# Optimization experiments

Measured on AMD Instinct MI355X. Metric: run time of the kernel, lower is better.

The kernel has to match this reference:

```python
import jax, jax.numpy as jnp
import numpy as np
from jax import lax

TOPN = 4
CAT_NUM = 4
NUM_CLS = 200
PAD = 224
IMG = 448
HP = IMG + 2 * PAD  # 896
CROP = 224
IOU_THRESH = 0.25


def _gen_edge_anchors():
    # generate_default_anchor_maps: 3 pyramid levels; anchors ordered (anchor, h, w)
    # per level to match the channel-first flatten of ProposalNet tidy outputs.
    settings = [
        (32, 48.0, [2 ** (1. / 3.), 2 ** (2. / 3.)], [0.667, 1.0, 1.5]),
        (64, 96.0, [2 ** (1. / 3.), 2 ** (2. / 3.)], [0.667, 1.0, 1.5]),
        (128, 192.0, [1.0, 2 ** (1. / 3.), 2 ** (2. / 3.)], [0.667, 1.0, 1.5]),
    ]
    blocks = []
    for stride, size, scales, ars in settings:
        n = int(np.ceil(IMG / stride))
        c = np.arange(n, dtype=np.float64) * stride + stride / 2.0
        cy, cx = np.meshgrid(c, c, indexing='ij')
        for sc in scales:
            for ar in ars:
                h = size * sc / np.sqrt(ar)
                w = size * sc * np.sqrt(ar)
                a = np.stack([cy - h / 2., cx - w / 2., cy + h / 2., cx + w / 2.], axis=-1)
                blocks.append(a.reshape(-1, 4))
    e = np.concatenate(blocks, axis=0)  # [1614, 4] (y0,x0,y1,x1)
    return (e + PAD).astype(np.int32)   # offset into padded image, truncated to int


EDGE_ANCHORS = _gen_edge_anchors()


def _conv(x, w, b, stride, pad):
    y = lax.conv_general_dilated(x, w, (stride, stride), [(pad, pad), (pad, pad)],
                                 dimension_numbers=('NCHW', 'OIHW', 'NCHW'))
    return y + b[None, :, None, None]


def _proposal_net(x, d1w, d1b, d2w, d2b, d3w, d3b, t1w, t1b, t2w, t2b, t3w, t3b):
    B = x.shape[0]
    d1 = jax.nn.relu(_conv(x, d1w, d1b, 1, 1))   # [B,128,14,14]
    d2 = jax.nn.relu(_conv(d1, d2w, d2b, 2, 1))  # [B,128,7,7]
    d3 = jax.nn.relu(_conv(d2, d3w, d3b, 2, 1))  # [B,128,4,4]
    t1 = _conv(d1, t1w, t1b, 1, 0).reshape(B, -1)  # 6*14*14 = 1176
    t2 = _conv(d2, t2w, t2b, 1, 0).reshape(B, -1)  # 6*7*7  = 294
    t3 = _conv(d3, t3w, t3b, 1, 0).reshape(B, -1)  # 9*4*4  = 144
    return jnp.concatenate([t1, t2, t3], axis=1)   # [B,1614]


def _hard_nms(scores, boxes, area):
    # Greedy hard NMS over A anchors, returns TOPN kept indices (score-desc order).
    A = scores.shape[0]

    def body(k, carry):
        mask, idxs = carry
        i = jnp.argmax(jnp.where(mask, scores, -jnp.inf))
        b = boxes[i]
        yy0 = jnp.maximum(boxes[:, 0], b[0])
        xx0 = jnp.maximum(boxes[:, 1], b[1])
        yy1 = jnp.minimum(boxes[:, 2], b[2])
        xx1 = jnp.minimum(boxes[:, 3], b[3])
        inter = jnp.maximum(yy1 - yy0, 0.) * jnp.maximum(xx1 - xx0, 0.)
        iou = inter / (area + area[i] - inter)
        mask = (mask & (iou < IOU_THRESH)).at[i].set(False)
        return mask, idxs.at[k].set(i.astype(jnp.int32))

    _, idxs = lax.fori_loop(0, TOPN, body, (jnp.ones((A,), bool), jnp.zeros((TOPN,), jnp.int32)))
    return idxs


def _crop_resize(img, box):
    # img [3,HP,HP], box [4] float (integer-valued). Bilinear, align_corners=True:
    # src coord = y0 + i*(h-1)/(CROP-1) over the slice [y0:y1).
    y0, x0, y1, x1 = box[0], box[1], box[2], box[3]
    t = jnp.arange(CROP, dtype=jnp.float32) / (CROP - 1.)
    ys = y0 + t * (y1 - y0 - 1.)
    xs = x0 + t * (x1 - x0 - 1.)
    yi0 = jnp.clip(jnp.floor(ys).astype(jnp.int32), 0, HP - 1)
    xi0 = jnp.clip(jnp.floor(xs).astype(jnp.int32), 0, HP - 1)
    yi1 = jnp.minimum(yi0 + 1, HP - 1)
    xi1 = jnp.minimum(xi0 + 1, HP - 1)
    wy = (ys - yi0.astype(jnp.float32))[None, :, None]
    wx = (xs - xi0.astype(jnp.float32))[None, None, :]
    r0 = img[:, yi0, :]
    r1 = img[:, yi1, :]
    rows = r0 + (r1 - r0) * wy          # [3,CROP,HP]
    c0 = rows[:, :, xi0]
    c1 = rows[:, :, xi1]
    return c0 + (c1 - c0) * wx          # [3,CROP,CROP]


def reference(x, rpn_feature, feature, resnet_out,
              down1_w, down1_b, down2_w, down2_b, down3_w, down3_b,
              tidy1_w, tidy1_b, tidy2_w, tidy2_b, tidy3_w, tidy3_b,
              feat_w, feat_b, partcls_w, partcls_b, concat_w, concat_b):
    B = x.shape[0]
    boxes_f = jnp.asarray(EDGE_ANCHORS, jnp.float32)
    area = (boxes_f[:, 2] - boxes_f[:, 0]) * (boxes_f[:, 3] - boxes_f[:, 1])

    rpn_score = _proposal_net(lax.stop_gradient(rpn_feature),
                              down1_w, down1_b, down2_w, down2_b, down3_w, down3_b,
                              tidy1_w, tidy1_b, tidy2_w, tidy2_b, tidy3_w, tidy3_b)
    scores_sg = lax.stop_gradient(rpn_score)
    top_idx = jax.vmap(lambda s: _hard_nms(s, boxes_f, area))(scores_sg)   # [B,TOPN]
    top_n_prob = jnp.take_along_axis(rpn_score, top_idx, axis=1)           # [B,TOPN]

    x_pad = jnp.pad(x, ((0, 0), (0, 0), (PAD, PAD), (PAD, PAD)))           # [B,3,896,896]
    sel_boxes = boxes_f[top_idx]                                           # [B,TOPN,4]
    part_imgs = jax.vmap(lambda img, bxs: jax.vmap(lambda b: _crop_resize(img, b))(bxs))(x_pad, sel_boxes)
    part_imgs = lax.stop_gradient(part_imgs).reshape(B * TOPN, 3, CROP, CROP)  # detach()

    # per-crop feature trunk (stand-in for shared ResNet50): strided 7x7 conv + GAP
    pf = jax.nn.relu(_conv(part_imgs, feat_w, feat_b, 32, 3)).mean(axis=(2, 3))  # [B*TOPN,2048]
    part_logits = (pf @ partcls_w.T + partcls_b).reshape(B, TOPN, NUM_CLS)
    part_feature = pf.reshape(B, TOPN, -1)[:, :CAT_NUM].reshape(B, -1)           # [B,4*2048]
    concat_out = jnp.concatenate([part_feature, feature], axis=1)                # [B,10240]
    concat_logits = concat_out @ concat_w.T + concat_b
    return resnet_out, concat_logits, part_logits, top_idx, top_n_prob


def setup_inputs():
    key = jax.random.key(0)
    ks = jax.random.split(key, 13)
    B = 16
    n = lambda k, shp, s=1.0: jax.random.normal(k, shp, jnp.float32) * s
    z = lambda c: jnp.zeros((c,), jnp.float32)
    return {
        'x': n(ks[0], (B, 3, 448, 448)),
        'rpn_feature': jax.nn.relu(n(ks[1], (B, 2048, 14, 14))),
        'feature': n(ks[2], (B, 2048)),
        'resnet_out': n(ks[3], (B, 200)),
        'down1_w': n(ks[4], (128, 2048, 3, 3), 0.01),
        'down1_b': z(128),
        'down2_w': n(ks[5], (128, 128, 3, 3), 0.03),
        'down2_b': z(128),
        'down3_w': n(ks[6], (128, 128, 3, 3), 0.03),
        'down3_b': z(128),
        'tidy1_w': n(ks[7], (6, 128, 1, 1), 0.1),
        'tidy1_b': z(6),
        'tidy2_w': n(ks[8], (6, 128, 1, 1), 0.1),
        'tidy2_b': z(6),
        'tidy3_w': n(ks[9], (9, 128, 1, 1), 0.1),
        'tidy3_b': z(9),
        'feat_w': n(ks[10], (2048, 3, 7, 7), 0.05),
        'feat_b': z(2048),
        'partcls_w': n(ks[11], (200, 2048), 0.02),
        'partcls_b': z(200),
        'concat_w': n(ks[12], (200, 2048 * (CAT_NUM + 1)), 0.01),
        'concat_b': z(200),
    }
```

## Files before the change

### kernel.cpp

```cpp
#include <hip/hip_runtime.h>
#include <math.h>

#define NANCH 1614
#define A1 1176
#define A2 1470
#define KSPLIT 4
#define N_D1E (16*128*196)

#define OFF_D1 0
#define OFF_D2 401408
#define OFF_D3 501760
#define OFF_SC 534528
#define OFF_PF 560352
#define OFF_P  691424
#define OFF_INT 1152416
#define OFF_BIG 1158944
#define SZ_AT 3211264
#define SZ_BW 1179648
#define OFF_ATH (OFF_BIG)
#define OFF_ATL (OFF_ATH + SZ_AT)
#define OFF_BWH (OFF_ATL + SZ_AT)
#define OFF_BWL (OFF_BWH + SZ_BW)
#define OFF_PM  (OFF_BWL + SZ_BW)
#define SZ_PM   3612672
#define TOTAL_MFMA_F (OFF_PM + SZ_PM)
#define N_D2E (16*128*49)
#define N_D3E (16*128*16)
#define OFF_P2 OFF_BIG
#define OFF_P3 (OFF_BIG + 4*N_D2E)

#define OUT_CONCAT 3200
#define OUT_PART   6400
#define OUT_TIDX   19200
#define OUT_TPROB  19264

typedef __attribute__((ext_vector_type(8))) short short8;
typedef __attribute__((ext_vector_type(4))) float f32x4;

__device__ __forceinline__ unsigned short bf16_rn(float f) {
    unsigned u = __float_as_uint(f);
    unsigned r = u + 0x7fffu + ((u >> 16) & 1u);
    return (unsigned short)(r >> 16);
}
__device__ __forceinline__ float bf16_to_f(unsigned short h) {
    return __uint_as_float(((unsigned)h) << 16);
}

__global__ void anchor_kernel(int* __restrict__ anc) {
    int i = blockIdx.x * 256 + threadIdx.x;
    if (i >= NANCH) return;
    int stride, n, sgroup, j;
    double size;
    if (i < A1)      { stride = 32;  size = 48.0;  n = 14; j = i;      sgroup = 0; }
    else if (i < A2) { stride = 64;  size = 96.0;  n = 7;  j = i - A1; sgroup = 0; }
    else             { stride = 128; size = 192.0; n = 4;  j = i - A2; sgroup = 1; }
    int cells = n * n;
    int combo = j / cells, cell = j % cells;
    int sc_i = combo / 3, ar_i = combo % 3;
    double sc;
    if (sgroup == 0) sc = pow(2.0, (double)(sc_i + 1) / 3.0);
    else             sc = (sc_i == 0) ? 1.0 : pow(2.0, (double)sc_i / 3.0);
    double ar = (ar_i == 0) ? 0.667 : ((ar_i == 1) ? 1.0 : 1.5);
    int y = cell / n, x = cell % n;
    double cy = (double)y * stride + stride / 2.0;
    double cx = (double)x * stride + stride / 2.0;
    double sq = sqrt(ar);
    double h = size * sc / sq, w = size * sc * sq;
    anc[i*4+0] = (int)(cy - h/2.0 + 224.0);
    anc[i*4+1] = (int)(cx - w/2.0 + 224.0);
    anc[i*4+2] = (int)(cy + h/2.0 + 224.0);
    anc[i*4+3] = (int)(cx + w/2.0 + 224.0);
}

__launch_bounds__(256)
__global__ void split_rpn_t(const float* __restrict__ rpn,
                            unsigned short* __restrict__ ath, unsigned short* __restrict__ atl) {
    __shared__ float T[32*197];
    int b = blockIdx.x >> 6, icb = blockIdx.x & 63;
    int tid = threadIdx.x;
    for (int idx = tid; idx < 32*196; idx += 256) {
        int i = idx / 196, s = idx % 196;
        T[i*197 + s] = rpn[((size_t)(b*2048 + icb*32 + i))*196 + s];
    }
    __syncthreads();
    for (int idx = tid; idx < 32*196; idx += 256) {
        int s = idx >> 5, i = idx & 31;
        float f = T[i*197 + s];
        unsigned short hi = bf16_rn(f);
        unsigned short lo = bf16_rn(f - bf16_to_f(hi));
        size_t o = ((size_t)(b*196 + s))*2048 + icb*32 + i;
        ath[o] = hi; atl[o] = lo;
    }
}

__global__ void split_w(const float* __restrict__ w1,
                        unsigned short* __restrict__ bwh, unsigned short* __restrict__ bwl) {
    int idx = blockIdx.x * 256 + threadIdx.x;
    if (idx >= 9*128*2048) return;
    int tap = idx / (128*2048);
    int rem = idx % (128*2048);
    int oc = rem >> 11, ic = rem & 2047;
    float f = w1[((size_t)(oc*2048 + ic))*9 + tap];
    unsigned short hi = bf16_rn(f);
    unsigned short lo = bf16_rn(f - bf16_to_f(hi));
    bwh[idx] = hi; bwl[idx] = lo;
}

#define ABUF (64*40)
#define BBUF (128*40)
__launch_bounds__(256)
__global__ void d1_mfma(const unsigned short* __restrict__ ath, const unsigned short* __restrict__ atl,
                        const unsigned short* __restrict__ bwh, const unsigned short* __restrict__ bwl,
                        float* __restrict__ partM) {
    __shared__ unsigned short Ah[2*ABUF], Al[2*ABUF], Bh[2*BBUF], Bl[2*BBUF];
    int tid = threadIdx.x;
    int tap = blockIdx.x / 49, mb = blockIdx.x % 49;
    int dy = tap/3 - 1, dx = tap%3 - 1;
    int wave = tid >> 6, lane = tid & 63;
    int wr = wave >> 1, wc = wave & 1;
    int lg = lane >> 4, lr = lane & 15;

    const unsigned short* asrc[2]; unsigned short* adst[2]; bool avalid[2];
#pragma unroll
    for (int rep = 0; rep < 2; ++rep) {
        int idx = rep*256 + tid;
        int rw = idx >> 3, half = (idx >> 2) & 1, slot = idx & 3;
        int grow = mb*64 + rw;
        int b = grow / 196, s = grow % 196;
        int y = s / 14, x = s % 14;
        int ys = y + dy, xs = x + dx;
        bool av = (ys >= 0) && (ys < 14) && (xs >= 0) && (xs < 14);
        avalid[rep] = av;
        asrc[rep] = (half ? atl : ath)
            + ((size_t)(b*196 + (av ? (ys*14 + xs) : 0)))*2048 + slot*8;
        adst[rep] = (half ? Al : Ah) + rw*40 + slot*8;
    }
    const unsigned short* bsrc[4]; unsigned short* bdst[4];
#pragma unroll
    for (int rep = 0; rep < 4; ++rep) {
        int idx = rep*256 + tid;
        int oc = idx >> 3, half = (idx >> 2) & 1, slot = idx & 3;
        bsrc[rep] = (half ? bwl : bwh) + ((size_t)(tap*128 + oc))*2048 + slot*8;
        bdst[rep] = (half ? Bl : Bh) + oc*40 + slot*8;
    }

    f32x4 acc[2][4];
#pragma unroll
    for (int r2 = 0; r2 < 2; ++r2)
#pragma unroll
        for (int f = 0; f < 4; ++f) acc[r2][f] = (f32x4){0.f, 0.f, 0.f, 0.f};
    const short8 zer = {0,0,0,0,0,0,0,0};

    short8 ga[2], gb[4];
#pragma unroll
    for (int rep = 0; rep < 2; ++rep) ga[rep] = avalid[rep] ? *(const short8*)(asrc[rep]) : zer;
#pragma unroll
    for (int rep = 0; rep < 4; ++rep) gb[rep] = *(const short8*)(bsrc[rep]);
#pragma unroll
    for (int rep = 0; rep < 2; ++rep) *(short8*)(adst[rep]) = ga[rep];
#pragma unroll
    for (int rep = 0; rep < 4; ++rep) *(short8*)(bdst[rep]) = gb[rep];
    __syncthreads();

    int abase_w = wr*32*40 + lr*40 + lg*8;
    int bbase_w = wc*64*40 + lg*8;

    for (int step = 0; step < 64; ++step) {
        int buf = step & 1;
        if (step + 1 < 64) {
            int ic0 = (step + 1) * 32;
#pragma unroll
            for (int rep = 0; rep < 2; ++rep) ga[rep] = avalid[rep] ? *(const short8*)(asrc[rep] + ic0) : zer;
#pragma unroll
            for (int rep = 0; rep < 4; ++rep) gb[rep] = *(const short8*)(bsrc[rep] + ic0);
        }
        int ab = buf*ABUF, bb = buf*BBUF;
        short8 ah0 = *(const short8*)&Ah[ab + abase_w];
        short8 ah1 = *(const short8*)&Ah[ab + abase_w + 16*40];
        short8 al0 = *(const short8*)&Al[ab + abase_w];
        short8 al1 = *(const short8*)&Al[ab + abase_w + 16*40];
#pragma unroll
        for (int f = 0; f < 4; ++f) {
            int bo = bb + bbase_w + (f*16 + lr)*40;
            short8 b_h = *(const short8*)&Bh[bo];
            short8 b_l = *(const short8*)&Bl[bo];
            acc[0][f] = __builtin_amdgcn_mfma_f32_16x16x32_bf16(ah0, b_h, acc[0][f], 0, 0, 0);
            acc[0][f] = __builtin_amdgcn_mfma_f32_16x16x32_bf16(ah0, b_l, acc[0][f], 0, 0, 0);
            acc[0][f] = __builtin_amdgcn_mfma_f32_16x16x32_bf16(al0, b_h, acc[0][f], 0, 0, 0);
            acc[1][f] = __builtin_amdgcn_mfma_f32_16x16x32_bf16(ah1, b_h, acc[1][f], 0, 0, 0);
            acc[1][f] = __builtin_amdgcn_mfma_f32_16x16x32_bf16(ah1, b_l, acc[1][f], 0, 0, 0);
            acc[1][f] = __builtin_amdgcn_mfma_f32_16x16x32_bf16(al1, b_h, acc[1][f], 0, 0, 0);
        }
        if (step + 1 < 64) {
            int nb = buf ^ 1;
#pragma unroll
            for (int rep = 0; rep < 2; ++rep) *(short8*)(adst[rep] + nb*ABUF) = ga[rep];
#pragma unroll
            for (int rep = 0; rep < 4; ++rep) *(short8*)(bdst[rep] + nb*BBUF) = gb[rep];
        }
        __syncthreads();
    }
#pragma unroll
    for (int r2 = 0; r2 < 2; ++r2)
#pragma unroll
    for (int f = 0; f < 4; ++f) {
        int oc = wc*64 + f*16 + lr;
#pragma unroll
        for (int r = 0; r < 4; ++r) {
            int row = mb*64 + wr*32 + r2*16 + lg*4 + r;
            partM[((size_t)tap*3136 + row)*128 + oc] = acc[r2][f][r];
        }
    }
}

__global__ void d1_combine(const float* __restrict__ partM, const float* __restrict__ b1,
                           float* __restrict__ d1) {
    int idx = blockIdx.x*256 + threadIdx.x;
    if (idx >= 3136*128) return;
    int oc = idx & 127, row = idx >> 7;
    float s = 0.f;
#pragma unroll
    for (int t = 0; t < 9; ++t) s += partM[(size_t)t*3136*128 + idx];
    int b = row / 196, sp = row % 196;
    d1[(b*128 + oc)*196 + sp] = fmaxf(s + b1[oc], 0.f);
}

__launch_bounds__(256)
__global__ void conv_d1_part(const float* __restrict__ rpn, const float* __restrict__ w1,
                             float* __restrict__ part) {
    __shared__ float lin[8*256];
    __shared__ float lwT[576];
    int tid = threadIdx.x;
    int ks = blockIdx.x & 3;
    int tile = (blockIdx.x >> 2) & 15;
    int b = blockIdx.x >> 6;
    int py = tid >> 4, px = tid & 15;
    bool pvalid = (py >= 1) && (py <= 14) && (px >= 1) && (px <= 14);
    int in_off = (b*2048)*196 + (py-1)*14 + (px-1);
    const float* wb = w1 + tile*8*18432;
    int s = tid, y = s / 14, x = s % 14;
    bool active = s < 196;
    float acc[8];
#pragma unroll
    for (int o = 0; o < 8; ++o) acc[o] = 0.f;
    float pv[8]; float wv[3];
    int c0 = ks * 64;
#pragma unroll
    for (int i = 0; i < 8; ++i) pv[i] = pvalid ? rpn[in_off + (c0*8 + i)*196] : 0.f;
#pragma unroll
    for (int r = 0; r < 3; ++r) {
        int u = tid + r*256;
        if (u < 576) { int oc = u/72, rem = u%72; wv[r] = wb[oc*18432 + c0*72 + rem]; }
    }
    for (int c = 0; c < 64; ++c) {
#pragma unroll
        for (int i = 0; i < 8; ++i) lin[i*256 + tid] = pv[i];
#pragma unroll
        for (int r = 0; r < 3; ++r) {
            int u = tid + r*256;
            if (u < 576) { int oc = u/72, rem = u%72; lwT[rem*8 + oc] = wv[r]; }
        }
        __syncthreads();
        if (c + 1 < 64) {
            int icb = (c0 + c + 1) * 8;
#pragma unroll
            for (int i = 0; i < 8; ++i) pv[i] = pvalid ? rpn[in_off + (icb + i)*196] : 0.f;
#pragma unroll
            for (int r = 0; r < 3; ++r) {
                int u = tid + r*256;
                if (u < 576) { int oc = u/72, rem = u%72; wv[r] = wb[oc*18432 + icb*9 + rem]; }
            }
        }
        if (active) {
#pragma unroll
            for (int ic = 0; ic < 8; ++ic) {
                int base = ic*256 + y*16 + x;
                float p[9];
                p[0]=lin[base+0];  p[1]=lin[base+1];  p[2]=lin[base+2];
                p[3]=lin[base+16]; p[4]=lin[base+17]; p[5]=lin[base+18];
                p[6]=lin[base+32]; p[7]=lin[base+33]; p[8]=lin[base+34];
#pragma unroll
                for (int k = 0; k < 9; ++k) {
                    const float4 wa  = *(const float4*)&lwT[(ic*9 + k)*8];
                    const float4 wb4 = *(const float4*)&lwT[(ic*9 + k)*8 + 4];
                    acc[0] += p[k]*wa.x;  acc[1] += p[k]*wa.y;
                    acc[2] += p[k]*wa.z;  acc[3] += p[k]*wa.w;
                    acc[4] += p[k]*wb4.x; acc[5] += p[k]*wb4.y;
                    acc[6] += p[k]*wb4.z; acc[7] += p[k]*wb4.w;
                }
            }
        }
        __syncthreads();
    }
    if (active) {
#pragma unroll
        for (int o = 0; o < 8; ++o) {
            int oc = tile*8 + o;
            part[ks*N_D1E + (b*128 + oc)*196 + s] = acc[o];
        }
    }
}

__global__ void d1_reduce(const float* __restrict__ part, const float* __restrict__ b1,
                          float* __restrict__ d1) {
    int idx = blockIdx.x * 256 + threadIdx.x;
    if (idx >= N_D1E) return;
    int oc = (idx / 196) & 127;
    float s = part[idx] + part[idx + N_D1E] + part[idx + 2*N_D1E] + part[idx + 3*N_D1E];
    d1[idx] = fmaxf(s + b1[oc], 0.f);
}

__launch_bounds__(256)
__global__ void conv_d2_part(const float* __restrict__ d1, const float* __restrict__ w2,
                             float* __restrict__ part) {
    __shared__ float lin[8*320];
    __shared__ float lwT[72*32];
    int tid = threadIdx.x;
    int ks = blockIdx.x & 3;
    int octile = (blockIdx.x >> 2) & 3;
    int b = blockIdx.x >> 4;
    int py = tid >> 4, px = tid & 15;
    bool pvalid = (py >= 1) && (py <= 14) && (px >= 1) && (px <= 14);
    int in_base = (b*128)*196 + (py-1)*14 + (px-1);
    int g = tid >> 6, s = tid & 63;
    int yo = s / 7, xo = s % 7;
    bool active = s < 49;
    const float* wb = w2 + (octile*32)*1152 + ks*288;

    float acc[8];
#pragma unroll
    for (int o = 0; o < 8; ++o) acc[o] = 0.f;
    float pv[8], wv[9];
#pragma unroll
    for (int i = 0; i < 8; ++i) pv[i] = pvalid ? d1[in_base + (ks*32 + i)*196] : 0.f;
#pragma unroll
    for (int r = 0; r < 9; ++r) {
        int u = tid + r*256; int oc_l = u/72, rem = u%72;
        wv[r] = wb[oc_l*1152 + rem];
    }
    for (int c = 0; c < 4; ++c) {
#pragma unroll
        for (int i = 0; i < 8; ++i) lin[i*320 + py*20 + px] = pv[i];
#pragma unroll
        for (int r = 0; r < 9; ++r) {
            int u = tid + r*256; int oc_l = u/72, rem = u%72;
            lwT[rem*32 + oc_l] = wv[r];
        }
        __syncthreads();
        if (c + 1 < 4) {
            int ic0 = ks*32 + (c+1)*8;
#pragma unroll
            for (int i = 0; i < 8; ++i) pv[i] = pvalid ? d1[in_base + (ic0 + i)*196] : 0.f;
#pragma unroll
            for (int r = 0; r < 9; ++r) {
                int u = tid + r*256; int oc_l = u/72, rem = u%72;
                wv[r] = wb[oc_l*1152 + (c+1)*72 + rem];
            }
        }
        if (active) {
#pragma unroll
            for (int ic = 0; ic < 8; ++ic) {
                int base = ic*320 + (2*yo)*20 + 2*xo;
                float p[9];
                p[0]=lin[base+0];  p[1]=lin[base+1];  p[2]=lin[base+2];
                p[3]=lin[base+20]; p[4]=lin[base+21]; p[5]=lin[base+22];
                p[6]=lin[base+40]; p[7]=lin[base+41]; p[8]=lin[base+42];
#pragma unroll
                for (int k = 0; k < 9; ++k) {
                    const float4 wa  = *(const float4*)&lwT[(ic*9 + k)*32 + g*8];
                    const float4 wb4 = *(const float4*)&lwT[(ic*9 + k)*32 + g*8 + 4];
                    acc[0] += p[k]*wa.x;  acc[1] += p[k]*wa.y;
                    acc[2] += p[k]*wa.z;  acc[3] += p[k]*wa.w;
                    acc[4] += p[k]*wb4.x; acc[5] += p[k]*wb4.y;
                    acc[6] += p[k]*wb4.z; acc[7] += p[k]*wb4.w;
                }
            }
        }
        __syncthreads();
    }
    if (active) {
#pragma unroll
        for (int o = 0; o < 8; ++o) {
            int oc = octile*32 + g*8 + o;
            part[ks*N_D2E + (b*128 + oc)*49 + s] = acc[o];
        }
    }
}

__launch_bounds__(256)
__global__ void conv_d3_part(const float* __restrict__ d2, const float* __restrict__ w3,
                             float* __restrict__ part) {
    __shared__ float lin3[8*108];
    __shared__ float lwT3[72*128];
    int tid = threadIdx.x;
    int ks = blockIdx.x & 15;
    int b = blockIdx.x >> 4;
    int g = tid >> 4, s = tid & 15;
    int yo = s >> 2, xo = s & 3;

    for (int r = 0; r < 4; ++r) {
        int u = tid + r*256;
        if (u < 864) {
            int ic = u / 108, rem = u % 108;
            int ty = rem / 12, tx = rem % 12;
            int iy = ty - 1, ix = tx - 1;
            float v = 0.f;
            if (iy >= 0 && iy < 7 && ix >= 0 && ix < 7)
                v = d2[(b*128 + ks*8 + ic)*49 + iy*7 + ix];
            lin3[u] = v;
        }
    }
#pragma unroll
    for (int r = 0; r < 36; ++r) {
        int u = tid + r*256;
        int oc_l = u / 72, rem = u % 72;
        lwT3[rem*128 + oc_l] = w3[oc_l*1152 + ks*72 + rem];
    }
    __syncthreads();

    float acc[8];
#pragma unroll
    for (int o = 0; o < 8; ++o) acc[o] = 0.f;
#pragma unroll
    for (int ic = 0; ic < 8; ++ic) {
        int base = ic*108 + (2*yo)*12 + 2*xo;
        float p[9];
        p[0]=lin3[base+0];  p[1]=lin3[base+1];  p[2]=lin3[base+2];
        p[3]=lin3[base+12]; p[4]=lin3[base+13]; p[5]=lin3[base+14];
        p[6]=lin3[base+24]; p[7]=lin3[base+25]; p[8]=lin3[base+26];
#pragma unroll
        for (int k = 0; k < 9; ++k) {
            const float4 wa  = *(const float4*)&lwT3[(ic*9 + k)*128 + g*8];
            const float4 wb4 = *(const float4*)&lwT3[(ic*9 + k)*128 + g*8 + 4];
            acc[0] += p[k]*wa.x;  acc[1] += p[k]*wa.y;
            acc[2] += p[k]*wa.z;  acc[3] += p[k]*wa.w;
            acc[4] += p[k]*wb4.x; acc[5] += p[k]*wb4.y;
            acc[6] += p[k]*wb4.z; acc[7] += p[k]*wb4.w;
        }
    }
#pragma unroll
    for (int o = 0; o < 8; ++o) {
        int oc = g*8 + o;
        part[ks*N_D3E + (b*128 + oc)*16 + s] = acc[o];
    }
}

__global__ void reduce_relu(const float* __restrict__ part, const float* __restrict__ bias,
                            float* __restrict__ out, int nsplit, int N, int SP) {
    int idx = blockIdx.x*256 + threadIdx.x;
    if (idx >= N) return;
    int oc = (idx / SP) & 127;
    float s = 0.f;
    for (int p = 0; p < nsplit; ++p) s += part[p*N + idx];
    out[idx] = fmaxf(s + bias[oc], 0.f);
}

__global__ void tidy_kernel(const float* __restrict__ d1, const float* __restrict__ d2, const float* __restrict__ d3,
                            const float* __restrict__ t1w, const float* __restrict__ t1b,
                            const float* __restrict__ t2w, const float* __restrict__ t2b,
                            const float* __restrict__ t3w, const float* __restrict__ t3b,
                            float* __restrict__ scores) {
    int idx = blockIdx.x * 256 + threadIdx.x;
    if (idx >= 16*NANCH) return;
    int b = idx / NANCH, i = idx % NANCH;
    const float* src; const float* tw; const float* tb; int S, c, s;
    if (i < A1)      { c = i/196;           s = i%196;        src = d1 + b*128*196 + s; S = 196; tw = t1w; tb = t1b; }
    else if (i < A2) { int j = i - A1; c = j/49; s = j%49;    src = d2 + b*128*49  + s; S = 49;  tw = t2w; tb = t2b; }
    else             { int j = i - A2; c = j/16; s = j%16;    src = d3 + b*128*16  + s; S = 16;  tw = t3w; tb = t3b; }
    float acc = tb[c];
    const float* wr = tw + c*128;
    for (int ic = 0; ic < 128; ++ic) acc += src[ic*S] * wr[ic];
    scores[idx] = acc;
}

__launch_bounds__(256)
__global__ void nms_kernel(const float* __restrict__ scores, const int* __restrict__ anc,
                           int* __restrict__ topidx, float* __restrict__ out) {
    __shared__ float s[NANCH];
    __shared__ float by0[NANCH], bx0[NANCH], by1[NANCH], bx1[NANCH], ar[NANCH];
    __shared__ float rv[256]; __shared__ int ri[256];
    __shared__ int sel[4];
    int b = blockIdx.x, tid = threadIdx.x;
    for (int j = tid; j < NANCH; j += 256) {
        s[j] = scores[b*NANCH + j];
        float y0 = (float)anc[j*4+0], x0 = (float)anc[j*4+1];
        float y1 = (float)anc[j*4+2], x1 = (float)anc[j*4+3];
        by0[j] = y0; bx0[j] = x0; by1[j] = y1; bx1[j] = x1;
        ar[j] = (y1 - y0) * (x1 - x0);
    }
    __syncthreads();
    for (int k = 0; k < 4; ++k) {
        float bv = -INFINITY; int bi = NANCH;
        for (int j = tid; j < NANCH; j += 256) {
            float v = s[j];
            if (v > bv) { bv = v; bi = j; }
        }
        rv[tid] = bv; ri[tid] = bi;
        __syncthreads();
        for (int off = 128; off > 0; off >>= 1) {
            if (tid < off) {
                float v2 = rv[tid+off]; int i2 = ri[tid+off];
                if (v2 > rv[tid] || (v2 == rv[tid] && i2 < ri[tid])) { rv[tid] = v2; ri[tid] = i2; }
            }
            __syncthreads();
        }
        int i = ri[0];
        if (tid == 0) sel[k] = i;
        float a0 = by0[i], a1 = bx0[i], a2 = by1[i], a3 = bx1[i], ai = ar[i];
        for (int j = tid; j < NANCH; j += 256) {
            float yy0 = fmaxf(by0[j], a0), xx0 = fmaxf(bx0[j], a1);
            float yy1 = fminf(by1[j], a2), xx1 = fminf(bx1[j], a3);
            float inter = fmaxf(yy1 - yy0, 0.f) * fmaxf(xx1 - xx0, 0.f);
            float iou = inter / (ar[j] + ai - inter);
            if (!(iou < 0.25f)) s[j] = -INFINITY;
        }
        if (tid == 0) s[i] = -INFINITY;
        __syncthreads();
    }
    if (tid < 4) {
        int i = sel[tid];
        topidx[b*4 + tid] = i;
        out[OUT_TIDX  + b*4 + tid] = (float)i;
        out[OUT_TPROB + b*4 + tid] = scores[b*NANCH + i];
    }
}

__device__ __forceinline__ float fetchpix(const float* img, int Y, int X) {
    if (Y >= 224 && Y < 672 && X >= 224 && X < 672) return img[(Y - 224)*448 + (X - 224)];
    return 0.f;
}

__global__ void sampler_kernel(const float* __restrict__ x, const int* __restrict__ anc,
                               const int* __restrict__ topidx, float* __restrict__ P) {
    int crop = blockIdx.x >> 2;
    int b = crop >> 2;
    int idx = topidx[crop];
    float y0 = (float)anc[idx*4+0], x0 = (float)anc[idx*4+1];
    float y1 = (float)anc[idx*4+2], x1 = (float)anc[idx*4+3];
    float dy = y1 - y0 - 1.0f, dx = x1 - x0 - 1.0f;
    const float* imgb = x + b*3*448*448;
    for (int u = (blockIdx.x & 3)*256 + threadIdx.x; u < 7203; u += 1024) {
        int c = u / 2401; int rem = u % 2401;
        int rid = rem / 49, cid = rem % 49;
        int oy = rid/7, ky = rid%7, ox = cid/7, kx = cid%7;
        int rr = 32*oy - 3 + ky, cc = 32*ox - 3 + kx;
        float val = 0.f;
        if (rr >= 0 && cc >= 0) {
            float ty = (float)rr / 223.0f;
            float ys = __fadd_rn(y0, __fmul_rn(ty, dy));
            int yi0 = (int)floorf(ys); yi0 = yi0 < 0 ? 0 : (yi0 > 895 ? 895 : yi0);
            int yi1 = (yi0 + 1 > 895) ? 895 : yi0 + 1;
            float wy = ys - (float)yi0;
            float tx = (float)cc / 223.0f;
            float xs = __fadd_rn(x0, __fmul_rn(tx, dx));
            int xi0 = (int)floorf(xs); xi0 = xi0 < 0 ? 0 : (xi0 > 895 ? 895 : xi0);
            int xi1 = (xi0 + 1 > 895) ? 895 : xi0 + 1;
            float wx = xs - (float)xi0;
            const float* img = imgb + c*448*448;
            float p00 = fetchpix(img, yi0, xi0), p10 = fetchpix(img, yi1, xi0);
            float p01 = fetchpix(img, yi0, xi1), p11 = fetchpix(img, yi1, xi1);
            float r0 = p00 + (p10 - p00)*wy;
            float r1 = p01 + (p11 - p01)*wy;
            val = r0 + (r1 - r0)*wx;
        }
        int pos = oy*7 + ox, kk = c*49 + ky*7 + kx;
        P[crop*7203 + pos*147 + kk] = val;
    }
}

__launch_bounds__(256)
__global__ void feat_gemm_kernel(const float* __restrict__ P, const float* __restrict__ fw,
                                 const float* __restrict__ fb, float* __restrict__ pf) {
    __shared__ float lp[49*148];
    int crop = blockIdx.x >> 3, tile = blockIdx.x & 7;
    int oc = tile*256 + threadIdx.x;
    for (int u = threadIdx.x; u < 7203; u += 256)
        lp[(u/147)*148 + (u%147)] = P[crop*7203 + u];
    __syncthreads();
    float s[49];
#pragma unroll
    for (int p = 0; p < 49; ++p) s[p] = 0.f;
    const float* wr = fw + oc*147;
    for (int kc = 0; kc < 36; ++kc) {
        float w0 = wr[kc*4], w1 = wr[kc*4+1], w2 = wr[kc*4+2], w3 = wr[kc*4+3];
#pragma unroll
        for (int p = 0; p < 49; ++p) {
            float4 v = *(const float4*)&lp[p*148 + kc*4];
            s[p] += v.x*w0 + v.y*w1 + v.z*w2 + v.w*w3;
        }
    }
    {
        float w0 = wr[144], w1 = wr[145], w2 = wr[146];
#pragma unroll
        for (int p = 0; p < 49; ++p)
            s[p] += lp[p*148+144]*w0 + lp[p*148+145]*w1 + lp[p*148+146]*w2;
    }
    float bias = fb[oc], acc = 0.f;
#pragma unroll
    for (int p = 0; p < 49; ++p) acc += fmaxf(s[p] + bias, 0.f);
    pf[crop*2048 + oc] = acc / 49.0f;
}

__global__ void partcls_kernel(const float* __restrict__ pf, const float* __restrict__ pw,
                               const float* __restrict__ pb, float* __restrict__ out) {
    int o = blockIdx.x; int crop = o / 200, cls = o % 200;
    int lane = threadIdx.x;
    const float* a = pf + crop*2048; const float* w = pw + cls*2048;
    float sum = 0.f;
#pragma unroll
    for (int i = 0; i < 8; ++i) {
        int k = lane*4 + i*256;
        float4 a4 = *(const float4*)&a[k];
        float4 w4 = *(const float4*)&w[k];
        sum += a4.x*w4.x + a4.y*w4.y + a4.z*w4.z + a4.w*w4.w;
    }
#pragma unroll
    for (int off = 32; off > 0; off >>= 1) sum += __shfl_down(sum, off);
    if (lane == 0) out[OUT_PART + o] = sum + pb[cls];
}

__launch_bounds__(256)
__global__ void concat_kernel(const float* __restrict__ pf, const float* __restrict__ feature,
                              const float* __restrict__ cw, const float* __restrict__ cb,
                              float* __restrict__ out) {
    __shared__ float red[4][16];
    int j = blockIdx.x, tid = threadIdx.x;
    const float* w = cw + (size_t)j*10240;
    float acc[16];
#pragma unroll
    for (int b = 0; b < 16; ++b) acc[b] = 0.f;
    for (int k = tid; k < 10240; k += 256) {
        float wk = w[k];
        const float* v; int stride;
        if (k < 8192) { v = pf + k; stride = 8192; }
        else          { v = feature + (k - 8192); stride = 2048; }
#pragma unroll
        for (int b = 0; b < 16; ++b) acc[b] += v[b*stride] * wk;
    }
#pragma unroll
    for (int b = 0; b < 16; ++b) {
        float s2 = acc[b];
#pragma unroll
        for (int off = 32; off > 0; off >>= 1) s2 += __shfl_down(s2, off);
        if ((tid & 63) == 0) red[tid >> 6][b] = s2;
    }
    __syncthreads();
    if (tid < 16)
        out[OUT_CONCAT + tid*200 + j] = red[0][tid] + red[1][tid] + red[2][tid] + red[3][tid] + cb[j];
}

extern "C" void kernel_launch(void* const* d_in, const int* in_sizes, int n_in,
                              void* d_out, int out_size, void* d_ws, size_t ws_size,
                              hipStream_t stream) {
    const float* x    = (const float*)d_in[0];
    const float* rpn  = (const float*)d_in[1];
    const float* feat = (const float*)d_in[2];
    const float* rout = (const float*)d_in[3];
    const float* d1w  = (const float*)d_in[4];
    const float* d1b  = (const float*)d_in[5];
    const float* d2w  = (const float*)d_in[6];
    const float* d2b  = (const float*)d_in[7];
    const float* d3w  = (const float*)d_in[8];
    const float* d3b  = (const float*)d_in[9];
    const float* t1w  = (const float*)d_in[10];
    const float* t1b  = (const float*)d_in[11];
    const float* t2w  = (const float*)d_in[12];
    const float* t2b  = (const float*)d_in[13];
    const float* t3w  = (const float*)d_in[14];
    const float* t3b  = (const float*)d_in[15];
    const float* fw   = (const float*)d_in[16];
    const float* fbb  = (const float*)d_in[17];
    const float* pw   = (const float*)d_in[18];
    const float* pb   = (const float*)d_in[19];
    const float* cw   = (const float*)d_in[20];
    const float* cb   = (const float*)d_in[21];
    float* out = (float*)d_out;
    float* wsf = (float*)d_ws;
    float* d1  = wsf + OFF_D1;
    float* d2  = wsf + OFF_D2;
    float* d3  = wsf + OFF_D3;
    float* sc  = wsf + OFF_SC;
    float* pfb = wsf + OFF_PF;
    float* P   = wsf + OFF_P;
    int* anc    = (int*)(wsf + OFF_INT);
    int* topidx = anc + NANCH*4;

    hipMemcpyAsync(out, rout, 3200*sizeof(float), hipMemcpyDeviceToDevice, stream);

    anchor_kernel<<<7, 256, 0, stream>>>(anc);

    bool use_mfma = ws_size >= (size_t)TOTAL_MFMA_F * sizeof(float);
    if (use_mfma) {
        unsigned short* ath = (unsigned short*)(wsf + OFF_ATH);
        unsigned short* atl = (unsigned short*)(wsf + OFF_ATL);
        unsigned short* bwh = (unsigned short*)(wsf + OFF_BWH);
        unsigned short* bwl = (unsigned short*)(wsf + OFF_BWL);
        float* pm = wsf + OFF_PM;
        split_rpn_t<<<1024, 256, 0, stream>>>(rpn, ath, atl);
        split_w<<<9216, 256, 0, stream>>>(d1w, bwh, bwl);
        d1_mfma<<<441, 256, 0, stream>>>(ath, atl, bwh, bwl, pm);
        d1_combine<<<(3136*128 + 255)/256, 256, 0, stream>>>(pm, d1b, d1);
    } else {
        float* part = wsf + OFF_BIG;
        conv_d1_part<<<16*16*KSPLIT, 256, 0, stream>>>(rpn, d1w, part);
        d1_reduce<<<(N_D1E + 255)/256, 256, 0, stream>>>(part, d1b, d1);
    }

    float* part2 = wsf + OFF_P2;
    float* part3 = wsf + OFF_P3;
    conv_d2_part<<<256, 256, 0, stream>>>(d1, d2w, part2);
    reduce_relu<<<(N_D2E + 255)/256, 256, 0, stream>>>(part2, d2b, d2, 4, N_D2E, 49);
    conv_d3_part<<<256, 256, 0, stream>>>(d2, d3w, part3);
    reduce_relu<<<(N_D3E + 255)/256, 256, 0, stream>>>(part3, d3b, d3, 16, N_D3E, 16);

    tidy_kernel<<<101, 256, 0, stream>>>(d1, d2, d3, t1w, t1b, t2w, t2b, t3w, t3b, sc);
    nms_kernel<<<16, 256, 0, stream>>>(sc, anc, topidx, out);
    sampler_kernel<<<256, 256, 0, stream>>>(x, anc, topidx, P);
    feat_gemm_kernel<<<512, 256, 0, stream>>>(P, fw, fbb, pfb);
    partcls_kernel<<<12800, 64, 0, stream>>>(pfb, pw, pb, out);
    concat_kernel<<<200, 256, 0, stream>>>(pfb, feat, cw, cb, out);
}
```

Baseline: 391.4 us.

## Port feature-conv GEMM to split-bf16 MFMA and swizzle d1 LDS layout

```diff
diff --git a/kernel.cpp b/kernel.cpp
--- a/kernel.cpp
+++ b/kernel.cpp
@@ -24,6 +24,10 @@
 #define OFF_PM  (OFF_BWL + SZ_BW)
 #define SZ_PM   3612672
 #define TOTAL_MFMA_F (OFF_PM + SZ_PM)
+#define OFF_BFH OFF_PM
+#define OFF_BFL (OFF_PM + 163840)
+#define OFF_PH  (OFF_PM + 327680)
+#define OFF_PL  (OFF_PM + 327680 + 250880)
 #define N_D2E (16*128*49)
 #define N_D3E (16*128*16)
 #define OFF_P2 OFF_BIG
@@ -106,19 +110,23 @@
     bwh[idx] = hi; bwl[idx] = lo;
 }
 
-#define ABUF (64*40)
-#define BBUF (128*40)
+#define ABUF 2048
+#define BBUF 4096
 __launch_bounds__(256)
 __global__ void d1_mfma(const unsigned short* __restrict__ ath, const unsigned short* __restrict__ atl,
                         const unsigned short* __restrict__ bwh, const unsigned short* __restrict__ bwl,
                         float* __restrict__ partM) {
     __shared__ unsigned short Ah[2*ABUF], Al[2*ABUF], Bh[2*BBUF], Bl[2*BBUF];
     int tid = threadIdx.x;
-    int tap = blockIdx.x / 49, mb = blockIdx.x % 49;
+    int q = blockIdx.x >> 3;
+    int tap = q / 7, g = q % 7;
+    int mb = g*8 + (blockIdx.x & 7);
+    if (mb >= 49) return;
     int dy = tap/3 - 1, dx = tap%3 - 1;
     int wave = tid >> 6, lane = tid & 63;
     int wr = wave >> 1, wc = wave & 1;
     int lg = lane >> 4, lr = lane & 15;
+    int ksw = (lg ^ (lr & 3)) << 3;
 
     const unsigned short* asrc[2]; unsigned short* adst[2]; bool avalid[2];
 #pragma unroll
@@ -133,7 +141,7 @@
         avalid[rep] = av;
         asrc[rep] = (half ? atl : ath)
             + ((size_t)(b*196 + (av ? (ys*14 + xs) : 0)))*2048 + slot*8;
-        adst[rep] = (half ? Al : Ah) + rw*40 + slot*8;
+        adst[rep] = (half ? Al : Ah) + rw*32 + ((slot ^ (rw & 3)) << 3);
     }
     const unsigned short* bsrc[4]; unsigned short* bdst[4];
 #pragma unroll
@@ -141,7 +149,7 @@
         int idx = rep*256 + tid;
         int oc = idx >> 3, half = (idx >> 2) & 1, slot = idx & 3;
         bsrc[rep] = (half ? bwl : bwh) + ((size_t)(tap*128 + oc))*2048 + slot*8;
-        bdst[rep] = (half ? Bl : Bh) + oc*40 + slot*8;
+        bdst[rep] = (half ? Bl : Bh) + oc*32 + ((slot ^ (oc & 3)) << 3);
     }
 
     f32x4 acc[2][4];
@@ -162,8 +170,8 @@
     for (int rep = 0; rep < 4; ++rep) *(short8*)(bdst[rep]) = gb[rep];
     __syncthreads();
 
-    int abase_w = wr*32*40 + lr*40 + lg*8;
-    int bbase_w = wc*64*40 + lg*8;
+    int arow0 = (wr*32 + lr)*32 + ksw;
+    int bbase = (wc*64 + lr)*32 + ksw;
 
     for (int step = 0; step < 64; ++step) {
         int buf = step & 1;
@@ -175,13 +183,13 @@
             for (int rep = 0; rep < 4; ++rep) gb[rep] = *(const short8*)(bsrc[rep] + ic0);
         }
         int ab = buf*ABUF, bb = buf*BBUF;
-        short8 ah0 = *(const short8*)&Ah[ab + abase_w];
-        short8 ah1 = *(const short8*)&Ah[ab + abase_w + 16*40];
-        short8 al0 = *(const short8*)&Al[ab + abase_w];
-        short8 al1 = *(const short8*)&Al[ab + abase_w + 16*40];
+        short8 ah0 = *(const short8*)&Ah[ab + arow0];
+        short8 ah1 = *(const short8*)&Ah[ab + arow0 + 16*32];
+        short8 al0 = *(const short8*)&Al[ab + arow0];
+        short8 al1 = *(const short8*)&Al[ab + arow0 + 16*32];
 #pragma unroll
         for (int f = 0; f < 4; ++f) {
-            int bo = bb + bbase_w + (f*16 + lr)*40;
+            int bo = bb + bbase + f*16*32;
             short8 b_h = *(const short8*)&Bh[bo];
             short8 b_l = *(const short8*)&Bl[bo];
             acc[0][f] = __builtin_amdgcn_mfma_f32_16x16x32_bf16(ah0, b_h, acc[0][f], 0, 0, 0);
@@ -530,6 +538,58 @@
     return 0.f;
 }
 
+__device__ __forceinline__ float sample_one(const float* imgb, int c, int rr, int cc,
+                                            float y0, float x0, float dy, float dx) {
+    float ty = (float)rr / 223.0f;
+    float ys = __fadd_rn(y0, __fmul_rn(ty, dy));
+    int yi0 = (int)floorf(ys); yi0 = yi0 < 0 ? 0 : (yi0 > 895 ? 895 : yi0);
+    int yi1 = (yi0 + 1 > 895) ? 895 : yi0 + 1;
+    float wy = ys - (float)yi0;
+    float tx = (float)cc / 223.0f;
+    float xs = __fadd_rn(x0, __fmul_rn(tx, dx));
+    int xi0 = (int)floorf(xs); xi0 = xi0 < 0 ? 0 : (xi0 > 895 ? 895 : xi0);
+    int xi1 = (xi0 + 1 > 895) ? 895 : xi0 + 1;
+    float wx = xs - (float)xi0;
+    const float* img = imgb + c*448*448;
+    float p00 = fetchpix(img, yi0, xi0), p10 = fetchpix(img, yi1, xi0);
+    float p01 = fetchpix(img, yi0, xi1), p11 = fetchpix(img, yi1, xi1);
+    float r0 = p00 + (p10 - p00)*wy;
+    float r1 = p01 + (p11 - p01)*wy;
+    return r0 + (r1 - r0)*wx;
+}
+
+__global__ void sampler_split_kernel(const float* __restrict__ x, const int* __restrict__ anc,
+                                     const int* __restrict__ topidx,
+                                     unsigned short* __restrict__ Ph, unsigned short* __restrict__ Pl) {
+    int crop = blockIdx.x >> 2;
+    int b = crop >> 2;
+    int idx = topidx[crop];
+    float y0 = (float)anc[idx*4+0], x0 = (float)anc[idx*4+1];
+    float y1 = (float)anc[idx*4+2], x1 = (float)anc[idx*4+3];
+    float dy = y1 - y0 - 1.0f, dx = x1 - x0 - 1.0f;
+    const float* imgb = x + b*3*448*448;
+    for (int u = (blockIdx.x & 3)*256 + threadIdx.x; u < 7203; u += 1024) {
+        int c = u / 2401; int rem = u % 2401;
+        int rid = rem / 49, cid = rem % 49;
+        int oy = rid/7, ky = rid%7, ox = cid/7, kx = cid%7;
+        int rr = 32*oy - 3 + ky, cc = 32*ox - 3 + kx;
+        float val = 0.f;
+        if (rr >= 0 && cc >= 0) val = sample_one(imgb, c, rr, cc, y0, x0, dy, dx);
+        int pos = oy*7 + ox, kk = c*49 + ky*7 + kx;
+        unsigned short hi = bf16_rn(val);
+        unsigned short lo = bf16_rn(val - bf16_to_f(hi));
+        size_t o = (size_t)crop*7840 + pos*160 + kk;
+        Ph[o] = hi; Pl[o] = lo;
+    }
+    if ((blockIdx.x & 3) == 0) {
+        for (int u = threadIdx.x; u < 49*13; u += 256) {
+            int pos = u / 13, kk = 147 + u % 13;
+            size_t o = (size_t)crop*7840 + pos*160 + kk;
+            Ph[o] = 0; Pl[o] = 0;
+        }
+    }
+}
+
 __global__ void sampler_kernel(const float* __restrict__ x, const int* __restrict__ anc,
                                const int* __restrict__ topidx, float* __restrict__ P) {
     int crop = blockIdx.x >> 2;
@@ -545,27 +605,122 @@
         int oy = rid/7, ky = rid%7, ox = cid/7, kx = cid%7;
         int rr = 32*oy - 3 + ky, cc = 32*ox - 3 + kx;
         float val = 0.f;
-        if (rr >= 0 && cc >= 0) {
-            float ty = (float)rr / 223.0f;
-            float ys = __fadd_rn(y0, __fmul_rn(ty, dy));
-            int yi0 = (int)floorf(ys); yi0 = yi0 < 0 ? 0 : (yi0 > 895 ? 895 : yi0);
-            int yi1 = (yi0 + 1 > 895) ? 895 : yi0 + 1;
-            float wy = ys - (float)yi0;
-            float tx = (float)cc / 223.0f;
-            float xs = __fadd_rn(x0, __fmul_rn(tx, dx));
-            int xi0 = (int)floorf(xs); xi0 = xi0 < 0 ? 0 : (xi0 > 895 ? 895 : xi0);
-            int xi1 = (xi0 + 1 > 895) ? 895 : xi0 + 1;
-            float wx = xs - (float)xi0;
-            const float* img = imgb + c*448*448;
-            float p00 = fetchpix(img, yi0, xi0), p10 = fetchpix(img, yi1, xi0);
-            float p01 = fetchpix(img, yi0, xi1), p11 = fetchpix(img, yi1, xi1);
-            float r0 = p00 + (p10 - p00)*wy;
-            float r1 = p01 + (p11 - p01)*wy;
-            val = r0 + (r1 - r0)*wx;
-        }
+        if (rr >= 0 && cc >= 0) val = sample_one(imgb, c, rr, cc, y0, x0, dy, dx);
         int pos = oy*7 + ox, kk = c*49 + ky*7 + kx;
         P[crop*7203 + pos*147 + kk] = val;
     }
+}
+
+__global__ void split_fw_kernel(const float* __restrict__ fw,
+                                unsigned short* __restrict__ bfh, unsigned short* __restrict__ bfl) {
+    int idx = blockIdx.x * 256 + threadIdx.x;
+    if (idx >= 2048*160) return;
+    int oc = idx / 160, k = idx % 160;
+    float f = (k < 147) ? fw[oc*147 + k] : 0.f;
+    unsigned short hi = bf16_rn(f);
+    unsigned short lo = bf16_rn(f - bf16_to_f(hi));
+    bfh[idx] = hi; bfl[idx] = lo;
+}
+
+#define FAB 2048
+#define FBB 4096
+__launch_bounds__(256)
+__global__ void feat_mfma(const unsigned short* __restrict__ Ph, const unsigned short* __restrict__ Pl,
+                          const unsigned short* __restrict__ Bfh, const unsigned short* __restrict__ Bfl,
+                          const float* __restrict__ fb, float* __restrict__ pf) {
+    __shared__ unsigned short Ah[FAB], Al[FAB], Bh[FBB], Bl[FBB];
+    __shared__ float red[2][128];
+    int tid = threadIdx.x;
+    int crop = blockIdx.x >> 4, octile = blockIdx.x & 15;
+    int wave = tid >> 6, lane = tid & 63;
+    int wr = wave >> 1, wc = wave & 1;
+    int lg = lane >> 4, lr = lane & 15;
+    int ksw = (lg ^ (lr & 3)) << 3;
+
+    const unsigned short* asrc[2]; unsigned short* adst[2]; bool avalid[2];
+#pragma unroll
+    for (int rep = 0; rep < 2; ++rep) {
+        int idx = rep*256 + tid;
+        int rw = idx >> 3, half = (idx >> 2) & 1, slot = idx & 3;
+        bool av = rw < 49;
+        avalid[rep] = av;
+        int rwc = av ? rw : 0;
+        asrc[rep] = (half ? Pl : Ph) + (size_t)crop*7840 + rwc*160 + slot*8;
+        adst[rep] = (half ? Al : Ah) + rw*32 + ((slot ^ (rw & 3)) << 3);
+    }
+    const unsigned short* bsrc[4]; unsigned short* bdst[4];
+#pragma unroll
+    for (int rep = 0; rep < 4; ++rep) {
+        int idx = rep*256 + tid;
+        int oc = idx >> 3, half = (idx >> 2) & 1, slot = idx & 3;
+        bsrc[rep] = (half ? Bfl : Bfh) + (size_t)(octile*128 + oc)*160 + slot*8;
+        bdst[rep] = (half ? Bl : Bh) + oc*32 + ((slot ^ (oc & 3)) << 3);
+    }
+
+    f32x4 acc[2][4];
+#pragma unroll
+    for (int r2 = 0; r2 < 2; ++r2)
+#pragma unroll
+        for (int f = 0; f < 4; ++f) acc[r2][f] = (f32x4){0.f, 0.f, 0.f, 0.f};
+    const short8 zer = {0,0,0,0,0,0,0,0};
+
+    int arow0 = (wr*32 + lr)*32 + ksw;
+    int bbase = (wc*64 + lr)*32 + ksw;
+
+    for (int step = 0; step < 5; ++step) {
+        int k0 = step*32;
+        short8 ga[2], gb[4];
+#pragma unroll
+        for (int rep = 0; rep < 2; ++rep) ga[rep] = avalid[rep] ? *(const short8*)(asrc[rep] + k0) : zer;
+#pragma unroll
+        for (int rep = 0; rep < 4; ++rep) gb[rep] = *(const short8*)(bsrc[rep] + k0);
+        __syncthreads();
+#pragma unroll
+        for (int rep = 0; rep < 2; ++rep) *(short8*)(adst[rep]) = ga[rep];
+#pragma unroll
+        for (int rep = 0; rep < 4; ++rep) *(short8*)(bdst[rep]) = gb[rep];
+        __syncthreads();
+        short8 ah0 = *(const short8*)&Ah[arow0];
+        short8 ah1 = *(const short8*)&Ah[arow0 + 16*32];
+        short8 al0 = *(const short8*)&Al[arow0];
+        short8 al1 = *(const short8*)&Al[arow0 + 16*32];
+#pragma unroll
+        for (int f = 0; f < 4; ++f) {
+            int bo = bbase + f*16*32;
+            short8 b_h = *(const short8*)&Bh[bo];
+            short8 b_l = *(const short8*)&Bl[bo];
+            acc[0][f] = __builtin_amdgcn_mfma_f32_16x16x32_bf16(ah0, b_h, acc[0][f], 0, 0, 0);
+            acc[0][f] = __builtin_amdgcn_mfma_f32_16x16x32_bf16(ah0, b_l, acc[0][f], 0, 0, 0);
+            acc[0][f] = __builtin_amdgcn_mfma_f32_16x16x32_bf16(al0, b_h, acc[0][f], 0, 0, 0);
+            acc[1][f] = __builtin_amdgcn_mfma_f32_16x16x32_bf16(ah1, b_h, acc[1][f], 0, 0, 0);
+            acc[1][f] = __builtin_amdgcn_mfma_f32_16x16x32_bf16(ah1, b_l, acc[1][f], 0, 0, 0);
+            acc[1][f] = __builtin_amdgcn_mfma_f32_16x16x32_bf16(al1, b_h, acc[1][f], 0, 0, 0);
+        }
+    }
+    float colsum[4];
+#pragma unroll
+    for (int f = 0; f < 4; ++f) {
+        float fbv = fb[octile*128 + wc*64 + f*16 + lr];
+        float s = 0.f;
+#pragma unroll
+        for (int r2 = 0; r2 < 2; ++r2)
+#pragma unroll
+        for (int r = 0; r < 4; ++r) {
+            int row = wr*32 + r2*16 + lg*4 + r;
+            float v = fmaxf(acc[r2][f][r] + fbv, 0.f);
+            if (row < 49) s += v;
+        }
+        s += __shfl_down(s, 32);
+        s += __shfl_down(s, 16);
+        colsum[f] = s;
+    }
+    if (lane < 16) {
+#pragma unroll
+        for (int f = 0; f < 4; ++f) red[wr][wc*64 + f*16 + lane] = colsum[f];
+    }
+    __syncthreads();
+    if (tid < 128)
+        pf[(size_t)crop*2048 + octile*128 + tid] = (red[0][tid] + red[1][tid]) * (1.0f/49.0f);
 }
 
 __launch_bounds__(256)
@@ -698,7 +853,7 @@
         float* pm = wsf + OFF_PM;
         split_rpn_t<<<1024, 256, 0, stream>>>(rpn, ath, atl);
         split_w<<<9216, 256, 0, stream>>>(d1w, bwh, bwl);
-        d1_mfma<<<441, 256, 0, stream>>>(ath, atl, bwh, bwl, pm);
+        d1_mfma<<<504, 256, 0, stream>>>(ath, atl, bwh, bwl, pm);
         d1_combine<<<(3136*128 + 255)/256, 256, 0, stream>>>(pm, d1b, d1);
     } else {
         float* part = wsf + OFF_BIG;
@@ -715,8 +870,20 @@
 
     tidy_kernel<<<101, 256, 0, stream>>>(d1, d2, d3, t1w, t1b, t2w, t2b, t3w, t3b, sc);
     nms_kernel<<<16, 256, 0, stream>>>(sc, anc, topidx, out);
-    sampler_kernel<<<256, 256, 0, stream>>>(x, anc, topidx, P);
-    feat_gemm_kernel<<<512, 256, 0, stream>>>(P, fw, fbb, pfb);
+
+    if (use_mfma) {
+        unsigned short* bfh = (unsigned short*)(wsf + OFF_BFH);
+        unsigned short* bfl = (unsigned short*)(wsf + OFF_BFL);
+        unsigned short* ph  = (unsigned short*)(wsf + OFF_PH);
+        unsigned short* pl  = (unsigned short*)(wsf + OFF_PL);
+        split_fw_kernel<<<1280, 256, 0, stream>>>(fw, bfh, bfl);
+        sampler_split_kernel<<<256, 256, 0, stream>>>(x, anc, topidx, ph, pl);
+        feat_mfma<<<1024, 256, 0, stream>>>(ph, pl, bfh, bfl, fbb, pfb);
+    } else {
+        sampler_kernel<<<256, 256, 0, stream>>>(x, anc, topidx, P);
+        feat_gemm_kernel<<<512, 256, 0, stream>>>(P, fw, fbb, pfb);
+    }
+
     partcls_kernel<<<12800, 64, 0, stream>>>(pfb, pw, pb, out);
     concat_kernel<<<200, 256, 0, stream>>>(pfb, feat, cw, cb, out);
 }
```

Result: faster. 336.6 us (-14.0%).
